# Kernel tuning notes

Measured on AMD Instinct MI355X. Metric: run time of the kernel, lower is better.

Reference implementation:

```python
import jax, jax.numpy as jnp
import numpy as np

B, C, H, W = 16, 64, 64, 64  # z_e shape; C == embedding_dim
K = 1024                     # num_embeddings
COMMITMENT_COST = 0.25
EPS = 1e-5


def setup_inputs() -> dict:
    key = jax.random.key(0)
    k1, k2 = jax.random.split(key)
    z_e = jax.random.normal(k1, (B, C, H, W), dtype=jnp.float32)
    # codebook init ~ U(-1/D, 1/D) as in the torch module
    emb_w = jax.random.uniform(k2, (K, C), dtype=jnp.float32, minval=-1.0 / C, maxval=1.0 / C)
    return {"z_e": z_e, "emb_w": emb_w}


def reference(z_e, emb_w):
    orig_dtype = z_e.dtype
    b, c, h, w = z_e.shape
    z = z_e.astype(jnp.float32)
    # per-channel std over (batch, h, w); computed under no_grad in torch -> stop_gradient
    std = jax.lax.stop_gradient(
        jnp.clip(jnp.std(z, axis=(0, 2, 3), keepdims=True, ddof=1), EPS, None)
    )
    z = z / std                                        # [b,c,h,w]
    zf = z.transpose(0, 2, 3, 1).reshape(-1, c)        # [N, c]
    ew = emb_w.astype(jnp.float32)                     # [K, c]
    # squared euclidean distances: ||z||^2 - 2 z.e + ||e||^2  -> [N, K]
    d = (
        jnp.sum(zf * zf, axis=1, keepdims=True)
        - 2.0 * (zf @ ew.T)
        + jnp.sum(ew * ew, axis=1)
    )
    idx = jnp.argmin(d, axis=1)                        # [N]
    z_q = ew[idx].reshape(b, h, w, c).transpose(0, 3, 1, 2)  # [b,c,h,w]
    z_sg = jax.lax.stop_gradient(z)
    commitment = COMMITMENT_COST * jnp.mean((z_sg - z_q) ** 2)
    codebook = jnp.mean((z_sg - z_q) ** 2)             # eval-mode codebook loss
    vq_loss = commitment + codebook
    z_q_st = (z + jax.lax.stop_gradient(z_q - z)).astype(orig_dtype)
    n_tokens = idx.shape[0]
    counts = jnp.zeros((K,), dtype=jnp.float32).at[idx].add(1.0)
    avg_probs = counts / n_tokens
    perplexity = jnp.exp(-jnp.sum(avg_probs * jnp.log(jnp.clip(avg_probs, 1e-10, None))))
    indices = idx.reshape(b, h, w)
    return z_q_st, vq_loss, perplexity, indices
```

## Files before the change

kernel.cpp:

```cpp
#include <hip/hip_runtime.h>
#include <math.h>
#include <float.h>

#define HW 4096
#define CHW 262144
#define NTOK 65536
#define NELEM 4194304

#define WS_LOSS 0
#define WS_STD  512
#define WS_EE   576
#define WS_E2   1600
#define WS_DONE 132672

#define EPSM 1.0e-4f

typedef __attribute__((ext_vector_type(8))) short bf16x8;
typedef __attribute__((ext_vector_type(4))) float f32x4;

__device__ __forceinline__ unsigned short f2bf(float x) {
  unsigned u = __float_as_uint(x);
  u += 0x7FFFu + ((u >> 16) & 1u);
  return (unsigned short)(u >> 16);
}
__device__ __forceinline__ float bf2f(unsigned short h) {
  return __uint_as_float(((unsigned)h) << 16);
}
__device__ __forceinline__ void gload_lds16(const unsigned short* g, unsigned short* l) {
  __builtin_amdgcn_global_load_lds(
      (const __attribute__((address_space(1))) unsigned int*)g,
      (__attribute__((address_space(3))) unsigned int*)l, 16, 0, 0);
}

__global__ __launch_bounds__(1024) void k_pre(const float* __restrict__ z,
                                              const float* __restrict__ emb,
                                              float* __restrict__ stdv,
                                              unsigned short* __restrict__ e2g,
                                              float* __restrict__ eeg,
                                              int* __restrict__ done) {
  __shared__ double rs[16], rs2[16];
  int tid = threadIdx.x;
  int blk = blockIdx.x;
  if (blk == 0 && tid == 0) *done = 0;
  if (blk < 64) {
    int c = blk;
    double s = 0.0, s2 = 0.0;
    const float* base = z + c * HW;
    #pragma unroll 4
    for (int jj = 0; jj < 16; ++jj) {
      int f = tid + (jj << 10);
      int b = f >> 10, off4 = f & 1023;
      float4 v = *(const float4*)(base + (size_t)b * CHW + (off4 << 2));
      s  += (double)v.x + (double)v.y + (double)v.z + (double)v.w;
      s2 += (double)v.x * v.x + (double)v.y * v.y + (double)v.z * v.z + (double)v.w * v.w;
    }
    for (int o = 32; o > 0; o >>= 1) {
      s += __shfl_down(s, o, 64);
      s2 += __shfl_down(s2, o, 64);
    }
    int wv = tid >> 6, ln = tid & 63;
    if (ln == 0) { rs[wv] = s; rs2[wv] = s2; }
    __syncthreads();
    if (tid == 0) {
      double S = 0.0, S2 = 0.0;
      #pragma unroll
      for (int w = 0; w < 16; ++w) { S += rs[w]; S2 += rs2[w]; }
      const double N = (double)NTOK;
      double var = (S2 - S * S / N) / (N - 1.0);
      float sd = (float)sqrt(var);
      stdv[c] = fmaxf(sd, 1e-5f);
    }
  } else {
    int ct = blk - 64;
    int k0 = ct << 6;
    int code = tid >> 4, c4 = tid & 15;
    float4 v = *(const float4*)(emb + (size_t)((k0 + code) << 6) + (c4 << 2));
    unsigned short h0 = f2bf(v.x), h1 = f2bf(v.y), h2 = f2bf(v.z), h3 = f2bf(v.w);
    unsigned short l0 = f2bf(v.x - bf2f(h0)), l1 = f2bf(v.y - bf2f(h1));
    unsigned short l2 = f2bf(v.z - bf2f(h2)), l3 = f2bf(v.w - bf2f(h3));
    int jL = (c4 >> 1) & 3;
    int e = (c4 & 1) << 2;
    int cH = code >> 4, cL = code & 15;
    size_t base = (size_t)ct * 8192 + cH * 512 + jL * 128 + cL * 8 + e;
    int jHh = c4 >> 3;
    *(uint2*)(e2g + base + (size_t)jHh * 2048) =
        make_uint2((unsigned)h0 | ((unsigned)h1 << 16), (unsigned)h2 | ((unsigned)h3 << 16));
    *(uint2*)(e2g + base + (size_t)(2 + jHh) * 2048) =
        make_uint2((unsigned)l0 | ((unsigned)l1 << 16), (unsigned)l2 | ((unsigned)l3 << 16));
    if (tid < 64) {
      const float* er = emb + (size_t)((k0 + tid) << 6);
      float s = 0.f;
      #pragma unroll
      for (int c = 0; c < 64; ++c) s = fmaf(er[c], er[c], s);
      eeg[k0 + tid] = s;
    }
  }
}

__global__ __launch_bounds__(256, 2) void k_vq(
    const float* __restrict__ z_e, const float* __restrict__ emb,
    const float* __restrict__ stdv, const float* __restrict__ eeg,
    const unsigned short* __restrict__ e2g,
    float* __restrict__ out_zq, float* __restrict__ out_idx,
    float* __restrict__ loss_part, int* __restrict__ done,
    float* __restrict__ out_scalars) {
  __shared__ unsigned short A2[16384];
  __shared__ unsigned short B2[16384];
  __shared__ double rl[4], rh[4];
  __shared__ int lastFlag;
  float* hs1 = (float*)A2;
  float* hs2 = (float*)A2 + 256;
  float* hs3 = (float*)A2 + 512;
  int*   hk1 = (int*)A2 + 768;
  int*   hk2 = (int*)A2 + 1024;
  int*   skf = (int*)A2 + 1280;
  int*   mk2f = (int*)A2 + 1408;
  int*   pairL = (int*)A2 + 1536;
  int*   fullL = (int*)A2 + 1664;
  int*   cntB = (int*)A2 + 1792;
  int*   cntC = (int*)A2 + 1793;
  float* sred = (float*)A2 + 1796;
  float* zf   = (float*)A2 + 1800;
  float* fbd4 = (float*)A2 + 1864;
  int*   fbk4 = (int*)A2 + 1868;
  int*   hist = (int*)A2 + 1872;

  int tid = threadIdx.x;
  int lane = tid & 63;
  int wv = tid >> 6;
  int blk = blockIdx.x;
  int b = blk >> 5;
  int s0 = (blk & 31) << 7;

  {
    int tok = tid >> 1, half = tid & 1;
    const float* zsrc = z_e + (size_t)b * CHW + (size_t)(half << 5) * HW + s0 + tok;
    unsigned hw_[16], lw_[16];
    #pragma unroll
    for (int cc = 0; cc < 32; ++cc) {
      float v = zsrc[(size_t)cc * HW] / stdv[(half << 5) + cc];
      unsigned short h = f2bf(v);
      unsigned short l = f2bf(v - bf2f(h));
      if (cc & 1) { hw_[cc >> 1] |= ((unsigned)h) << 16; lw_[cc >> 1] |= ((unsigned)l) << 16; }
      else        { hw_[cc >> 1] = h;                    lw_[cc >> 1] = l; }
    }
    int tH = tok >> 4, tL = tok & 15;
    int base = tH * 512 + tL * 8;
    #pragma unroll
    for (int jj = 0; jj < 4; ++jj) {
      *(uint4*)(A2 + half * 4096 + base + jj * 128) =
          make_uint4(hw_[4 * jj], hw_[4 * jj + 1], hw_[4 * jj + 2], hw_[4 * jj + 3]);
      *(uint4*)(A2 + (2 + half) * 4096 + base + jj * 128) =
          make_uint4(lw_[4 * jj], lw_[4 * jj + 1], lw_[4 * jj + 2], lw_[4 * jj + 3]);
    }
  }

  int quad = lane >> 4, l15 = lane & 15;
  int wt = wv >> 1, wc = wv & 1;

  {
    const unsigned short* gsrc = e2g + wv * 512 + (lane << 3);
    unsigned short* ldst = B2 + wv * 512;
    #pragma unroll
    for (int rr = 0; rr < 4; ++rr)
      gload_lds16(gsrc + rr * 2048, ldst + rr * 2048);
  }
  __syncthreads();

  bf16x8 afc[4][4];
  #pragma unroll
  for (int j = 0; j < 4; ++j)
    #pragma unroll
    for (int mt = 0; mt < 4; ++mt)
      afc[j][mt] = *(const bf16x8*)(A2 + j * 4096 + ((wt << 2) + mt) * 512 + quad * 128 + l15 * 8);

  float ts1[16], ts2[16], ts3[16];
  int tk1[16], tk2[16];
  #pragma unroll
  for (int i = 0; i < 16; ++i) { ts1[i] = FLT_MAX; ts2[i] = FLT_MAX; ts3[i] = FLT_MAX; tk1[i] = 0; tk2[i] = 0; }

  const int aJH[8] = {0, 1, 2, 3, 0, 1, 2, 3};
  const int bJH[8] = {0, 1, 0, 1, 2, 3, 2, 3};

  #pragma unroll 1
  for (int ct = 0; ct < 16; ++ct) {
    const unsigned short* bb = B2 + (ct & 1) * 8192;
    if (ct < 15) {
      const unsigned short* gsrc = e2g + (size_t)(ct + 1) * 8192 + wv * 512 + (lane << 3);
      unsigned short* ldst = B2 + ((ct + 1) & 1) * 8192 + wv * 512;
      #pragma unroll
      for (int rr = 0; rr < 4; ++rr)
        gload_lds16(gsrc + rr * 2048, ldst + rr * 2048);
    }
    float ee0 = eeg[(ct << 6) + (wc << 5) + l15];
    float ee1 = eeg[(ct << 6) + (wc << 5) + 16 + l15];

    f32x4 acc[4][2];
    #pragma unroll
    for (int mt = 0; mt < 4; ++mt) { acc[mt][0] = (f32x4)(0.f); acc[mt][1] = (f32x4)(0.f); }

    #pragma unroll
    for (int s = 0; s < 8; ++s) {
      bf16x8 bfr[2];
      #pragma unroll
      for (int nt = 0; nt < 2; ++nt)
        bfr[nt] = *(const bf16x8*)(bb + bJH[s] * 2048 + ((wc << 1) + nt) * 512 + quad * 128 + l15 * 8);
      #pragma unroll
      for (int mt = 0; mt < 4; ++mt)
        #pragma unroll
        for (int nt = 0; nt < 2; ++nt)
          acc[mt][nt] = __builtin_amdgcn_mfma_f32_16x16x32_bf16(afc[aJH[s]][mt], bfr[nt], acc[mt][nt], 0, 0, 0);
    }

    #pragma unroll
    for (int nt = 0; nt < 2; ++nt) {
      int kc = (ct << 6) + (wc << 5) + (nt << 4) + l15;
      float eev = nt ? ee1 : ee0;
      #pragma unroll
      for (int mt = 0; mt < 4; ++mt) {
        #pragma unroll
        for (int r = 0; r < 4; ++r) {
          float sv = fmaf(-2.0f, acc[mt][nt][r], eev);
          int sl = (mt << 2) + r;
          bool lt1 = sv < ts1[sl];
          bool lt2 = sv < ts2[sl];
          bool lt3 = sv < ts3[sl];
          ts3[sl] = lt2 ? ts2[sl] : (lt3 ? sv : ts3[sl]);
          tk2[sl] = lt1 ? tk1[sl] : (lt2 ? kc : tk2[sl]);
          ts2[sl] = lt1 ? ts1[sl] : (lt2 ? sv : ts2[sl]);
          tk1[sl] = lt1 ? kc : tk1[sl];
          ts1[sl] = lt1 ? sv : ts1[sl];
        }
      }
    }
    if (ct < 15) __syncthreads();
  }
  __syncthreads();

  #pragma unroll
  for (int m = 1; m <= 8; m <<= 1) {
    #pragma unroll
    for (int sl = 0; sl < 16; ++sl) {
      float ob1 = __shfl_xor(ts1[sl], m, 64); int oq1 = __shfl_xor(tk1[sl], m, 64);
      float ob2 = __shfl_xor(ts2[sl], m, 64); int oq2 = __shfl_xor(tk2[sl], m, 64);
      float ob3 = __shfl_xor(ts3[sl], m, 64);
      bool t1 = (ts1[sl] < ob1) || (ts1[sl] == ob1 && tk1[sl] < oq1);
      float o1 = t1 ? ts1[sl] : ob1; int ok1 = t1 ? tk1[sl] : oq1;
      float aH = t1 ? ts2[sl] : ts1[sl]; int aHk = t1 ? tk2[sl] : tk1[sl]; float aH2 = t1 ? ts3[sl] : ts2[sl];
      float bH = t1 ? ob1 : ob2;         int bHk = t1 ? oq1 : oq2;         float bH2 = t1 ? ob2 : ob3;
      bool t2 = (aH < bH) || (aH == bH && aHk < bHk);
      float o2 = t2 ? aH : bH; int ok2 = t2 ? aHk : bHk;
      float aI = t2 ? aH2 : aH;
      float bI = t2 ? bH : bH2;
      ts1[sl] = o1; tk1[sl] = ok1; ts2[sl] = o2; tk2[sl] = ok2; ts3[sl] = fminf(aI, bI);
    }
  }
  if (tid == 0) { *cntB = 0; *cntC = 0; }
  if (l15 == 0) {
    #pragma unroll
    for (int mt = 0; mt < 4; ++mt)
      #pragma unroll
      for (int r = 0; r < 4; ++r) {
        int t = (wt << 6) + (mt << 4) + (quad << 2) + r;
        int sl = (mt << 2) + r;
        hs1[(wc << 7) + t] = ts1[sl]; hs2[(wc << 7) + t] = ts2[sl]; hs3[(wc << 7) + t] = ts3[sl];
        hk1[(wc << 7) + t] = tk1[sl]; hk2[(wc << 7) + t] = tk2[sl];
      }
  }
  __syncthreads();

  if (tid < 128) {
    float a1 = hs1[tid], a2 = hs2[tid], a3 = hs3[tid];
    int e1 = hk1[tid], e2 = hk2[tid];
    float b1 = hs1[128 + tid], b2 = hs2[128 + tid], b3 = hs3[128 + tid];
    int f1 = hk1[128 + tid], f2 = hk2[128 + tid];
    bool t1 = (a1 < b1) || (a1 == b1 && e1 < f1);
    float o1 = t1 ? a1 : b1; int ok1 = t1 ? e1 : f1;
    float aH = t1 ? a2 : a1; int aHk = t1 ? e2 : e1; float aH2 = t1 ? a3 : a2;
    float bH = t1 ? b1 : b2; int bHk = t1 ? f1 : f2; float bH2 = t1 ? b2 : b3;
    bool t2 = (aH < bH) || (aH == bH && aHk < bHk);
    float o2 = t2 ? aH : bH; int ok2 = t2 ? aHk : bHk;
    float o3 = fminf(t2 ? aH2 : aH, t2 ? bH : bH2);
    skf[tid] = ok1;
    mk2f[tid] = ok2;
    if (o2 - o1 <= EPSM) {
      if (o3 - o1 > EPSM) { int p = atomicAdd(cntB, 1); pairL[p] = tid; }
      else                { int p = atomicAdd(cntC, 1); fullL[p] = tid; }
    }
  }
  __syncthreads();

  int nB = *cntB, nC = *cntC;

  if (tid < nB) {
    int t = pairL[tid];
    int ka = skf[t], kb = mk2f[t];
    const float* za = z_e + (size_t)b * CHW + s0 + t;
    const float* ea = emb + ((size_t)ka << 6);
    const float* ebp = emb + ((size_t)kb << 6);
    float zz = 0.f, da = 0.f, db = 0.f;
    #pragma unroll
    for (int c = 0; c < 64; ++c) {
      float zv = za[(size_t)c * HW] / stdv[c];
      zz = fmaf(zv, zv, zz);
      da = fmaf(ea[c], zv, da);
      db = fmaf(ebp[c], zv, db);
    }
    float d1 = (zz - 2.0f * da) + eeg[ka];
    float d2 = (zz - 2.0f * db) + eeg[kb];
    if (d2 < d1 || (d2 == d1 && kb < ka)) skf[t] = kb;
  }
  __syncthreads();

  for (int i = 0; i < nC; ++i) {
    int t = fullL[i];
    if (tid < 64) zf[tid] = z_e[(size_t)b * CHW + (size_t)tid * HW + s0 + t] / stdv[tid];
    __syncthreads();
    const float4* zf4 = (const float4*)zf;
    const float* er0 = emb + ((size_t)(tid << 2) << 6);
    float zz = 0.f;
    float dot[4] = {0.f, 0.f, 0.f, 0.f};
    #pragma unroll
    for (int c4 = 0; c4 < 16; ++c4) {
      float4 zv = zf4[c4];
      zz = fmaf(zv.x, zv.x, zz); zz = fmaf(zv.y, zv.y, zz);
      zz = fmaf(zv.z, zv.z, zz); zz = fmaf(zv.w, zv.w, zz);
      #pragma unroll
      for (int j = 0; j < 4; ++j) {
        float4 ev = *(const float4*)(er0 + (j << 6) + (c4 << 2));
        dot[j] = fmaf(ev.x, zv.x, dot[j]);
        dot[j] = fmaf(ev.y, zv.y, dot[j]);
        dot[j] = fmaf(ev.z, zv.z, dot[j]);
        dot[j] = fmaf(ev.w, zv.w, dot[j]);
      }
    }
    float bdl = FLT_MAX; int bkl = 0;
    #pragma unroll
    for (int j = 0; j < 4; ++j) {
      float dd = (zz - 2.0f * dot[j]) + eeg[(tid << 2) + j];
      if (dd < bdl) { bdl = dd; bkl = (tid << 2) + j; }
    }
    #pragma unroll
    for (int m = 1; m <= 32; m <<= 1) {
      float od = __shfl_xor(bdl, m, 64);
      int   ok = __shfl_xor(bkl, m, 64);
      if (od < bdl || (od == bdl && ok < bkl)) { bdl = od; bkl = ok; }
    }
    if (lane == 0) { fbd4[wv] = bdl; fbk4[wv] = bkl; }
    __syncthreads();
    if (tid == 0) {
      float bb2 = fbd4[0]; int kk2 = fbk4[0];
      #pragma unroll
      for (int w = 1; w < 4; ++w)
        if (fbd4[w] < bb2 || (fbd4[w] == bb2 && fbk4[w] < kk2)) { bb2 = fbd4[w]; kk2 = fbk4[w]; }
      skf[t] = kk2;
    }
    __syncthreads();
  }
  __syncthreads();

  if (tid < 128) out_idx[(blk << 7) + tid] = (float)skf[tid];

  {
    int t = tid & 127;
    int ch = tid >> 7;
    int kq = skf[t];
    const float* eq = emb + ((size_t)kq << 6) + (ch << 5);
    const float* zb2 = z_e + (size_t)b * CHW + s0 + t;
    float* ob = out_zq + (size_t)b * CHW + s0 + t;
    float lsum = 0.f;
    #pragma unroll
    for (int jj = 0; jj < 32; ++jj) {
      int c = (ch << 5) + jj;
      float zv = zb2[(size_t)c * HW] / stdv[c];
      float e = eq[jj];
      float df = zv - e;
      lsum = fmaf(df, df, lsum);
      ob[(size_t)c * HW] = zv + (e - zv);
    }
    for (int o = 32; o > 0; o >>= 1) lsum += __shfl_down(lsum, o, 64);
    if (lane == 0) sred[wv] = lsum;
  }
  __syncthreads();

  if (tid == 0) {
    loss_part[blk] = sred[0] + sred[1] + sred[2] + sred[3];
    __threadfence();
    int prev = atomicAdd(done, 1);
    lastFlag = (prev == 511);
  }
  __syncthreads();
  if (!lastFlag) return;

  #pragma unroll
  for (int jj = 0; jj < 4; ++jj) hist[tid + (jj << 8)] = 0;
  __syncthreads();
  {
    const float2* idx2 = (const float2*)out_idx;
    for (int i = tid; i < NTOK / 2; i += 256) {
      float2 v = idx2[i];
      atomicAdd(&hist[(int)v.x], 1);
      atomicAdd(&hist[(int)v.y], 1);
    }
  }
  __syncthreads();
  double ls = (double)loss_part[tid] + (double)loss_part[tid + 256];
  double hsum = 0.0;
  #pragma unroll
  for (int jj = 0; jj < 4; ++jj) {
    float p = (float)hist[tid + (jj << 8)] * (1.0f / 65536.0f);
    float lg = logf(fmaxf(p, 1e-10f));
    hsum += (double)(p * lg);
  }
  for (int o = 32; o > 0; o >>= 1) {
    ls += __shfl_down(ls, o, 64);
    hsum += __shfl_down(hsum, o, 64);
  }
  if (lane == 0) { rl[wv] = ls; rh[wv] = hsum; }
  __syncthreads();
  if (tid == 0) {
    double L = rl[0] + rl[1] + rl[2] + rl[3];
    double Hn = rh[0] + rh[1] + rh[2] + rh[3];
    float m = (float)(L / (double)NELEM);
    out_scalars[0] = 0.25f * m + m;
    out_scalars[1] = expf((float)(-Hn));
  }
}

extern "C" void kernel_launch(void* const* d_in, const int* in_sizes, int n_in,
                              void* d_out, int out_size, void* d_ws, size_t ws_size,
                              hipStream_t stream) {
  const float* z_e = (const float*)d_in[0];
  const float* emb = (const float*)d_in[1];
  float* ws = (float*)d_ws;
  float* loss_part = ws + WS_LOSS;
  float* stdv = ws + WS_STD;
  float* eeg = ws + WS_EE;
  unsigned short* e2g = (unsigned short*)(ws + WS_E2);
  int* done = (int*)(ws + WS_DONE);

  float* out = (float*)d_out;
  float* out_zq = out;
  float* out_scalars = out + NELEM;
  float* out_idx = out + NELEM + 2;

  k_pre<<<80, 1024, 0, stream>>>(z_e, emb, stdv, e2g, eeg, done);
  k_vq<<<512, 256, 0, stream>>>(z_e, emb, stdv, eeg, e2g, out_zq, out_idx,
                                loss_part, done, out_scalars);
}
```

Baseline: 190.8 us.

## Halve VQ tile to 64 tokens, split std reduction, fuse histogram into blocks

The main kernel now processes 64 tokens per block instead of 128, which doubles the grid to 1024 blocks. LDS drops to 32 KB, with the A buffer reused as a second B buffer, and the occupancy hint rises to 3 blocks per SM. Each wave owns a 16-code slice, so the 4-way top-3 merge now runs in LDS. The per-channel std reduction is split across 4x more pre-kernel blocks, with the partial sums finalized in each VQ block. Division by std is replaced by multiplying with a reciprocal. The histogram is built with global atomics per block instead of a serial pass in the last block. This trades more redundant per-block work, such as reloading the A fragments and finalizing std, for better parallelism and a shorter tail.

Measured after the change: 372.3 us. 1.95x slower.

```diff
diff --git a/kernel.cpp b/kernel.cpp
--- a/kernel.cpp
+++ b/kernel.cpp
@@ -8,10 +8,11 @@
 #define NELEM 4194304
 
 #define WS_LOSS 0
-#define WS_STD  512
-#define WS_EE   576
-#define WS_E2   1600
-#define WS_DONE 132672
+#define WS_PART 1024
+#define WS_EE   2048
+#define WS_E2   3072
+#define WS_HIST 68608
+#define WS_DONE 69632
 
 #define EPSM 1.0e-4f
 
@@ -34,23 +35,23 @@
 
 __global__ __launch_bounds__(1024) void k_pre(const float* __restrict__ z,
                                               const float* __restrict__ emb,
-                                              float* __restrict__ stdv,
+                                              double* __restrict__ part,
                                               unsigned short* __restrict__ e2g,
                                               float* __restrict__ eeg,
+                                              int* __restrict__ hist,
                                               int* __restrict__ done) {
   __shared__ double rs[16], rs2[16];
   int tid = threadIdx.x;
   int blk = blockIdx.x;
   if (blk == 0 && tid == 0) *done = 0;
-  if (blk < 64) {
-    int c = blk;
+  if (blk < 256) {
+    int c = blk & 63, q = blk >> 6;
     double s = 0.0, s2 = 0.0;
-    const float* base = z + c * HW;
-    #pragma unroll 4
-    for (int jj = 0; jj < 16; ++jj) {
-      int f = tid + (jj << 10);
-      int b = f >> 10, off4 = f & 1023;
-      float4 v = *(const float4*)(base + (size_t)b * CHW + (off4 << 2));
+    const float* base = z + (size_t)c * HW;
+    #pragma unroll
+    for (int jj = 0; jj < 4; ++jj) {
+      int bb = (q << 2) + jj;
+      float4 v = *(const float4*)(base + (size_t)bb * CHW + (tid << 2));
       s  += (double)v.x + (double)v.y + (double)v.z + (double)v.w;
       s2 += (double)v.x * v.x + (double)v.y * v.y + (double)v.z * v.z + (double)v.w * v.w;
     }
@@ -65,13 +66,12 @@
       double S = 0.0, S2 = 0.0;
       #pragma unroll
       for (int w = 0; w < 16; ++w) { S += rs[w]; S2 += rs2[w]; }
-      const double N = (double)NTOK;
-      double var = (S2 - S * S / N) / (N - 1.0);
-      float sd = (float)sqrt(var);
-      stdv[c] = fmaxf(sd, 1e-5f);
+      part[(c << 2) + q] = S;
+      part[256 + (c << 2) + q] = S2;
     }
   } else {
-    int ct = blk - 64;
+    int ct = blk - 256;
+    if (ct == 0) hist[tid] = 0;
     int k0 = ct << 6;
     int code = tid >> 4, c4 = tid & 15;
     float4 v = *(const float4*)(emb + (size_t)((k0 + code) << 6) + (c4 << 2));
@@ -97,15 +97,16 @@
   }
 }
 
-__global__ __launch_bounds__(256, 2) void k_vq(
+__global__ __launch_bounds__(256, 3) void k_vq(
     const float* __restrict__ z_e, const float* __restrict__ emb,
-    const float* __restrict__ stdv, const float* __restrict__ eeg,
+    const double* __restrict__ part, const float* __restrict__ eeg,
     const unsigned short* __restrict__ e2g,
     float* __restrict__ out_zq, float* __restrict__ out_idx,
     float* __restrict__ loss_part, int* __restrict__ done,
-    float* __restrict__ out_scalars) {
-  __shared__ unsigned short A2[16384];
-  __shared__ unsigned short B2[16384];
+    float* __restrict__ out_scalars, int* __restrict__ hist) {
+  __shared__ unsigned short A2[8192];
+  __shared__ unsigned short B2[8192];
+  __shared__ float sRstd[64];
   __shared__ double rl[4], rh[4];
   __shared__ int lastFlag;
   float* hs1 = (float*)A2;
@@ -114,49 +115,61 @@
   int*   hk1 = (int*)A2 + 768;
   int*   hk2 = (int*)A2 + 1024;
   int*   skf = (int*)A2 + 1280;
-  int*   mk2f = (int*)A2 + 1408;
-  int*   pairL = (int*)A2 + 1536;
-  int*   fullL = (int*)A2 + 1664;
-  int*   cntB = (int*)A2 + 1792;
-  int*   cntC = (int*)A2 + 1793;
-  float* sred = (float*)A2 + 1796;
-  float* zf   = (float*)A2 + 1800;
-  float* fbd4 = (float*)A2 + 1864;
-  int*   fbk4 = (int*)A2 + 1868;
-  int*   hist = (int*)A2 + 1872;
+  int*   mk2f = (int*)A2 + 1344;
+  int*   pairL = (int*)A2 + 1408;
+  int*   fullL = (int*)A2 + 1472;
+  int*   cntB = (int*)A2 + 1536;
+  int*   cntC = (int*)A2 + 1537;
+  float* sred = (float*)A2 + 1540;
+  float* zf   = (float*)A2 + 1544;
+  float* fbd4 = (float*)A2 + 1608;
+  int*   fbk4 = (int*)A2 + 1612;
 
   int tid = threadIdx.x;
   int lane = tid & 63;
   int wv = tid >> 6;
   int blk = blockIdx.x;
-  int b = blk >> 5;
-  int s0 = (blk & 31) << 7;
+  int b = blk >> 6;
+  int s0 = (blk & 63) << 6;
+
+  if (tid < 64) {
+    double S = 0.0, S2 = 0.0;
+    #pragma unroll
+    for (int q = 0; q < 4; ++q) {
+      S += part[(tid << 2) + q];
+      S2 += part[256 + (tid << 2) + q];
+    }
+    const double N = (double)NTOK;
+    double var = (S2 - S * S / N) / (N - 1.0);
+    float sd = fmaxf((float)sqrt(var), 1e-5f);
+    sRstd[tid] = 1.0f / sd;
+  }
+  __syncthreads();
 
   {
-    int tok = tid >> 1, half = tid & 1;
-    const float* zsrc = z_e + (size_t)b * CHW + (size_t)(half << 5) * HW + s0 + tok;
-    unsigned hw_[16], lw_[16];
-    #pragma unroll
-    for (int cc = 0; cc < 32; ++cc) {
-      float v = zsrc[(size_t)cc * HW] / stdv[(half << 5) + cc];
+    int t = tid & 63, q = tid >> 6;
+    int half = q >> 1, jl0 = (q & 1) << 1;
+    const float* zsrc = z_e + (size_t)b * CHW + (size_t)(q << 4) * HW + s0 + t;
+    unsigned hw_[8], lw_[8];
+    #pragma unroll
+    for (int cc = 0; cc < 16; ++cc) {
+      float v = zsrc[(size_t)cc * HW] * sRstd[(q << 4) + cc];
       unsigned short h = f2bf(v);
       unsigned short l = f2bf(v - bf2f(h));
       if (cc & 1) { hw_[cc >> 1] |= ((unsigned)h) << 16; lw_[cc >> 1] |= ((unsigned)l) << 16; }
       else        { hw_[cc >> 1] = h;                    lw_[cc >> 1] = l; }
     }
-    int tH = tok >> 4, tL = tok & 15;
-    int base = tH * 512 + tL * 8;
-    #pragma unroll
-    for (int jj = 0; jj < 4; ++jj) {
-      *(uint4*)(A2 + half * 4096 + base + jj * 128) =
-          make_uint4(hw_[4 * jj], hw_[4 * jj + 1], hw_[4 * jj + 2], hw_[4 * jj + 3]);
-      *(uint4*)(A2 + (2 + half) * 4096 + base + jj * 128) =
-          make_uint4(lw_[4 * jj], lw_[4 * jj + 1], lw_[4 * jj + 2], lw_[4 * jj + 3]);
+    int base = (t >> 4) * 512 + (t & 15) * 8;
+    #pragma unroll
+    for (int u = 0; u < 2; ++u) {
+      *(uint4*)(A2 + half * 2048 + base + (jl0 + u) * 128) =
+          make_uint4(hw_[4 * u], hw_[4 * u + 1], hw_[4 * u + 2], hw_[4 * u + 3]);
+      *(uint4*)(A2 + (2 + half) * 2048 + base + (jl0 + u) * 128) =
+          make_uint4(lw_[4 * u], lw_[4 * u + 1], lw_[4 * u + 2], lw_[4 * u + 3]);
     }
   }
 
   int quad = lane >> 4, l15 = lane & 15;
-  int wt = wv >> 1, wc = wv & 1;
 
   {
     const unsigned short* gsrc = e2g + wv * 512 + (lane << 3);
@@ -172,7 +185,8 @@
   for (int j = 0; j < 4; ++j)
     #pragma unroll
     for (int mt = 0; mt < 4; ++mt)
-      afc[j][mt] = *(const bf16x8*)(A2 + j * 4096 + ((wt << 2) + mt) * 512 + quad * 128 + l15 * 8);
+      afc[j][mt] = *(const bf16x8*)(A2 + j * 2048 + mt * 512 + quad * 128 + l15 * 8);
+  __syncthreads();
 
   float ts1[16], ts2[16], ts3[16];
   int tk1[16], tk2[16];
@@ -184,53 +198,43 @@
 
   #pragma unroll 1
   for (int ct = 0; ct < 16; ++ct) {
-    const unsigned short* bb = B2 + (ct & 1) * 8192;
+    const unsigned short* bb = (ct & 1) ? A2 : B2;
     if (ct < 15) {
       const unsigned short* gsrc = e2g + (size_t)(ct + 1) * 8192 + wv * 512 + (lane << 3);
-      unsigned short* ldst = B2 + ((ct + 1) & 1) * 8192 + wv * 512;
+      unsigned short* ldst = (((ct + 1) & 1) ? A2 : B2) + wv * 512;
       #pragma unroll
       for (int rr = 0; rr < 4; ++rr)
         gload_lds16(gsrc + rr * 2048, ldst + rr * 2048);
     }
-    float ee0 = eeg[(ct << 6) + (wc << 5) + l15];
-    float ee1 = eeg[(ct << 6) + (wc << 5) + 16 + l15];
-
-    f32x4 acc[4][2];
-    #pragma unroll
-    for (int mt = 0; mt < 4; ++mt) { acc[mt][0] = (f32x4)(0.f); acc[mt][1] = (f32x4)(0.f); }
+    float ee0 = eeg[(ct << 6) + (wv << 4) + l15];
+
+    f32x4 acc[4];
+    #pragma unroll
+    for (int mt = 0; mt < 4; ++mt) acc[mt] = (f32x4)(0.f);
 
     #pragma unroll
     for (int s = 0; s < 8; ++s) {
-      bf16x8 bfr[2];
-      #pragma unroll
-      for (int nt = 0; nt < 2; ++nt)
-        bfr[nt] = *(const bf16x8*)(bb + bJH[s] * 2048 + ((wc << 1) + nt) * 512 + quad * 128 + l15 * 8);
+      bf16x8 bfr = *(const bf16x8*)(bb + bJH[s] * 2048 + wv * 512 + quad * 128 + l15 * 8);
       #pragma unroll
       for (int mt = 0; mt < 4; ++mt)
-        #pragma unroll
-        for (int nt = 0; nt < 2; ++nt)
-          acc[mt][nt] = __builtin_amdgcn_mfma_f32_16x16x32_bf16(afc[aJH[s]][mt], bfr[nt], acc[mt][nt], 0, 0, 0);
-    }
-
-    #pragma unroll
-    for (int nt = 0; nt < 2; ++nt) {
-      int kc = (ct << 6) + (wc << 5) + (nt << 4) + l15;
-      float eev = nt ? ee1 : ee0;
-      #pragma unroll
-      for (int mt = 0; mt < 4; ++mt) {
-        #pragma unroll
-        for (int r = 0; r < 4; ++r) {
-          float sv = fmaf(-2.0f, acc[mt][nt][r], eev);
-          int sl = (mt << 2) + r;
-          bool lt1 = sv < ts1[sl];
-          bool lt2 = sv < ts2[sl];
-          bool lt3 = sv < ts3[sl];
-          ts3[sl] = lt2 ? ts2[sl] : (lt3 ? sv : ts3[sl]);
-          tk2[sl] = lt1 ? tk1[sl] : (lt2 ? kc : tk2[sl]);
-          ts2[sl] = lt1 ? ts1[sl] : (lt2 ? sv : ts2[sl]);
-          tk1[sl] = lt1 ? kc : tk1[sl];
-          ts1[sl] = lt1 ? sv : ts1[sl];
-        }
+        acc[mt] = __builtin_amdgcn_mfma_f32_16x16x32_bf16(afc[aJH[s]][mt], bfr, acc[mt], 0, 0, 0);
+    }
+
+    int kc = (ct << 6) + (wv << 4) + l15;
+    #pragma unroll
+    for (int mt = 0; mt < 4; ++mt) {
+      #pragma unroll
+      for (int r = 0; r < 4; ++r) {
+        float sv = fmaf(-2.0f, acc[mt][r], ee0);
+        int sl = (mt << 2) + r;
+        bool lt1 = sv < ts1[sl];
+        bool lt2 = sv < ts2[sl];
+        bool lt3 = sv < ts3[sl];
+        ts3[sl] = lt2 ? ts2[sl] : (lt3 ? sv : ts3[sl]);
+        tk2[sl] = lt1 ? tk1[sl] : (lt2 ? kc : tk2[sl]);
+        ts2[sl] = lt1 ? ts1[sl] : (lt2 ? sv : ts2[sl]);
+        tk1[sl] = lt1 ? kc : tk1[sl];
+        ts1[sl] = lt1 ? sv : ts1[sl];
       }
     }
     if (ct < 15) __syncthreads();
@@ -261,30 +265,34 @@
     for (int mt = 0; mt < 4; ++mt)
       #pragma unroll
       for (int r = 0; r < 4; ++r) {
-        int t = (wt << 6) + (mt << 4) + (quad << 2) + r;
+        int t = (mt << 4) + (quad << 2) + r;
         int sl = (mt << 2) + r;
-        hs1[(wc << 7) + t] = ts1[sl]; hs2[(wc << 7) + t] = ts2[sl]; hs3[(wc << 7) + t] = ts3[sl];
-        hk1[(wc << 7) + t] = tk1[sl]; hk2[(wc << 7) + t] = tk2[sl];
+        hs1[(wv << 6) + t] = ts1[sl]; hs2[(wv << 6) + t] = ts2[sl]; hs3[(wv << 6) + t] = ts3[sl];
+        hk1[(wv << 6) + t] = tk1[sl]; hk2[(wv << 6) + t] = tk2[sl];
       }
   }
   __syncthreads();
 
-  if (tid < 128) {
+  if (tid < 64) {
     float a1 = hs1[tid], a2 = hs2[tid], a3 = hs3[tid];
-    int e1 = hk1[tid], e2 = hk2[tid];
-    float b1 = hs1[128 + tid], b2 = hs2[128 + tid], b3 = hs3[128 + tid];
-    int f1 = hk1[128 + tid], f2 = hk2[128 + tid];
-    bool t1 = (a1 < b1) || (a1 == b1 && e1 < f1);
-    float o1 = t1 ? a1 : b1; int ok1 = t1 ? e1 : f1;
-    float aH = t1 ? a2 : a1; int aHk = t1 ? e2 : e1; float aH2 = t1 ? a3 : a2;
-    float bH = t1 ? b1 : b2; int bHk = t1 ? f1 : f2; float bH2 = t1 ? b2 : b3;
-    bool t2 = (aH < bH) || (aH == bH && aHk < bHk);
-    float o2 = t2 ? aH : bH; int ok2 = t2 ? aHk : bHk;
-    float o3 = fminf(t2 ? aH2 : aH, t2 ? bH : bH2);
-    skf[tid] = ok1;
-    mk2f[tid] = ok2;
-    if (o2 - o1 <= EPSM) {
-      if (o3 - o1 > EPSM) { int p = atomicAdd(cntB, 1); pairL[p] = tid; }
+    int e1 = hk1[tid], e2v = hk2[tid];
+    #pragma unroll
+    for (int w = 1; w < 4; ++w) {
+      float b1 = hs1[(w << 6) + tid], b2 = hs2[(w << 6) + tid], b3 = hs3[(w << 6) + tid];
+      int f1 = hk1[(w << 6) + tid], f2 = hk2[(w << 6) + tid];
+      bool t1 = (a1 < b1) || (a1 == b1 && e1 < f1);
+      float o1 = t1 ? a1 : b1; int ok1 = t1 ? e1 : f1;
+      float aH = t1 ? a2 : a1; int aHk = t1 ? e2v : e1; float aH2 = t1 ? a3 : a2;
+      float bH = t1 ? b1 : b2; int bHk = t1 ? f1 : f2; float bH2 = t1 ? b2 : b3;
+      bool t2 = (aH < bH) || (aH == bH && aHk < bHk);
+      a1 = o1; e1 = ok1;
+      a2 = t2 ? aH : bH; e2v = t2 ? aHk : bHk;
+      a3 = fminf(t2 ? aH2 : aH, t2 ? bH : bH2);
+    }
+    skf[tid] = e1;
+    mk2f[tid] = e2v;
+    if (a2 - a1 <= EPSM) {
+      if (a3 - a1 > EPSM) { int p = atomicAdd(cntB, 1); pairL[p] = tid; }
       else                { int p = atomicAdd(cntC, 1); fullL[p] = tid; }
     }
   }
@@ -301,7 +309,7 @@
     float zz = 0.f, da = 0.f, db = 0.f;
     #pragma unroll
     for (int c = 0; c < 64; ++c) {
-      float zv = za[(size_t)c * HW] / stdv[c];
+      float zv = za[(size_t)c * HW] * sRstd[c];
       zz = fmaf(zv, zv, zz);
       da = fmaf(ea[c], zv, da);
       db = fmaf(ebp[c], zv, db);
@@ -314,7 +322,7 @@
 
   for (int i = 0; i < nC; ++i) {
     int t = fullL[i];
-    if (tid < 64) zf[tid] = z_e[(size_t)b * CHW + (size_t)tid * HW + s0 + t] / stdv[tid];
+    if (tid < 64) zf[tid] = z_e[(size_t)b * CHW + (size_t)tid * HW + s0 + t] * sRstd[tid];
     __syncthreads();
     const float4* zf4 = (const float4*)zf;
     const float* er0 = emb + ((size_t)(tid << 2) << 6);
@@ -359,24 +367,32 @@
   }
   __syncthreads();
 
-  if (tid < 128) out_idx[(blk << 7) + tid] = (float)skf[tid];
+  if (tid < 64) {
+    int k = skf[tid];
+    out_idx[(blk << 6) + tid] = (float)k;
+    atomicAdd(&hist[k], 1);
+  }
 
   {
-    int t = tid & 127;
-    int ch = tid >> 7;
+    int t = tid & 63;
+    int g = tid >> 6;
     int kq = skf[t];
-    const float* eq = emb + ((size_t)kq << 6) + (ch << 5);
-    const float* zb2 = z_e + (size_t)b * CHW + s0 + t;
-    float* ob = out_zq + (size_t)b * CHW + s0 + t;
+    const float* eq = emb + ((size_t)kq << 6) + (g << 4);
+    const float* zb2 = z_e + (size_t)b * CHW + (size_t)(g << 4) * HW + s0 + t;
+    float* ob = out_zq + (size_t)b * CHW + (size_t)(g << 4) * HW + s0 + t;
     float lsum = 0.f;
     #pragma unroll
-    for (int jj = 0; jj < 32; ++jj) {
-      int c = (ch << 5) + jj;
-      float zv = zb2[(size_t)c * HW] / stdv[c];
-      float e = eq[jj];
-      float df = zv - e;
-      lsum = fmaf(df, df, lsum);
-      ob[(size_t)c * HW] = zv + (e - zv);
+    for (int j4 = 0; j4 < 4; ++j4) {
+      float4 ev = *(const float4*)(eq + (j4 << 2));
+      #pragma unroll
+      for (int u = 0; u < 4; ++u) {
+        int jj = (j4 << 2) + u;
+        float zv = zb2[(size_t)jj * HW] * sRstd[(g << 4) + jj];
+        float e = (&ev.x)[u];
+        float df = zv - e;
+        lsum = fmaf(df, df, lsum);
+        ob[(size_t)jj * HW] = zv + (e - zv);
+      }
     }
     for (int o = 32; o > 0; o >>= 1) lsum += __shfl_down(lsum, o, 64);
     if (lane == 0) sred[wv] = lsum;
@@ -387,24 +403,13 @@
     loss_part[blk] = sred[0] + sred[1] + sred[2] + sred[3];
     __threadfence();
     int prev = atomicAdd(done, 1);
-    lastFlag = (prev == 511);
+    lastFlag = (prev == 1023);
   }
   __syncthreads();
   if (!lastFlag) return;
 
-  #pragma unroll
-  for (int jj = 0; jj < 4; ++jj) hist[tid + (jj << 8)] = 0;
-  __syncthreads();
-  {
-    const float2* idx2 = (const float2*)out_idx;
-    for (int i = tid; i < NTOK / 2; i += 256) {
-      float2 v = idx2[i];
-      atomicAdd(&hist[(int)v.x], 1);
-      atomicAdd(&hist[(int)v.y], 1);
-    }
-  }
-  __syncthreads();
-  double ls = (double)loss_part[tid] + (double)loss_part[tid + 256];
+  double ls = (double)loss_part[tid] + (double)loss_part[tid + 256]
+            + (double)loss_part[tid + 512] + (double)loss_part[tid + 768];
   double hsum = 0.0;
   #pragma unroll
   for (int jj = 0; jj < 4; ++jj) {
@@ -434,9 +439,10 @@
   const float* emb = (const float*)d_in[1];
   float* ws = (float*)d_ws;
   float* loss_part = ws + WS_LOSS;
-  float* stdv = ws + WS_STD;
+  double* part = (double*)(ws + WS_PART);
   float* eeg = ws + WS_EE;
   unsigned short* e2g = (unsigned short*)(ws + WS_E2);
+  int* hist = (int*)(ws + WS_HIST);
   int* done = (int*)(ws + WS_DONE);
 
   float* out = (float*)d_out;
@@ -444,7 +450,7 @@
   float* out_scalars = out + NELEM;
   float* out_idx = out + NELEM + 2;
 
-  k_pre<<<80, 1024, 0, stream>>>(z_e, emb, stdv, e2g, eeg, done);
-  k_vq<<<512, 256, 0, stream>>>(z_e, emb, stdv, eeg, e2g, out_zq, out_idx,
-                                loss_part, done, out_scalars);
-}
+  k_pre<<<272, 1024, 0, stream>>>(z_e, emb, part, e2g, eeg, hist, done);
+  k_vq<<<1024, 256, 0, stream>>>(z_e, emb, part, eeg, e2g, out_zq, out_idx,
+                                 loss_part, done, out_scalars, hist);
+}
```
